# Kernel tuning notes

Measured on AMD Instinct MI355X. Metric: run time of the kernel, lower is better.

The kernel has to match this reference:

```python
import jax, jax.numpy as jnp
import numpy as np
from jax import lax

B, H7, W24 = 2048, 7, 24

def _conv(x, w):
    # x: [B,Cin,H,W], w: [Cout,Cin,3,3], stride 1, SAME padding (= padding 1)
    return lax.conv_general_dilated(x, w, (1, 1), 'SAME',
                                    dimension_numbers=('NCHW', 'OIHW', 'NCHW'))

def _cell(x, h, c, Wx, bx, Wh, Wc):
    # Wx: [4H,Cin,3,3] (gates i,f,c,o fused), Wh: [4H,H,3,3], Wc: [3,1,H,Hh,Ww] peepholes (i,f,o)
    H = h.shape[1]
    g = _conv(x, Wx) + bx[None, :, None, None] + _conv(h, Wh)  # [B,4H,Hh,Ww]
    gi, gf, gc, go = jnp.split(g, 4, axis=1)
    ci = jax.nn.sigmoid(gi + c * Wc[0])
    cf = jax.nn.sigmoid(gf + c * Wc[1])
    cc = cf * c + ci * jnp.tanh(gc)
    co = jax.nn.sigmoid(go + cc * Wc[2])
    ch = co * jnp.tanh(cc)
    return ch, cc

def setup_inputs() -> dict:
    key = jax.random.key(0)
    ks = jax.random.split(key, 12)
    s = 0.05
    return {
        'input': jax.random.normal(ks[0], (B, 2, H7, W24), jnp.float32),
        'x_ex': jax.random.normal(ks[1], (B, W24), jnp.float32),
        'Wx0': jax.random.normal(ks[2], (128, 2, 3, 3), jnp.float32) * s,
        'bx0': jax.random.normal(ks[3], (128,), jnp.float32) * s,
        'Wh0': jax.random.normal(ks[4], (128, 32, 3, 3), jnp.float32) * s,
        'Wc0': jnp.zeros((3, 1, 32, H7, W24), jnp.float32),
        'Wx1': jax.random.normal(ks[5], (256, 32, 3, 3), jnp.float32) * s,
        'bx1': jax.random.normal(ks[6], (256,), jnp.float32) * s,
        'Wh1': jax.random.normal(ks[7], (256, 64, 3, 3), jnp.float32) * s,
        'Wc1': jnp.zeros((3, 1, 64, H7, W24), jnp.float32),
        'fc1_w': jax.random.normal(ks[8], (64, 64 * H7 * W24), jnp.float32) * s,
        'fc1_b': jax.random.normal(ks[9], (64,), jnp.float32) * s,
        'exfc_w': jax.random.normal(ks[10], (64, W24), jnp.float32) * s,
        'exfc_b': jax.random.normal(ks[11], (64,), jnp.float32) * s,
    }

def reference(input, x_ex, Wx0, bx0, Wh0, Wc0, Wx1, bx1, Wh1, Wc1,
              fc1_w, fc1_b, exfc_w, exfc_b):
    b = input.shape[0]
    z0 = jnp.zeros((b, 32, H7, W24), input.dtype)
    z1 = jnp.zeros((b, 64, H7, W24), input.dtype)

    def step_fn(carry, _):
        h0, c0, h1, c1 = carry
        h0, c0 = _cell(input, h0, c0, Wx0, bx0, Wh0, Wc0)
        h1, c1 = _cell(h0, h1, c1, Wx1, bx1, Wh1, Wc1)
        return (h0, c0, h1, c1), None

    (h0, c0, h1, c1), _ = lax.scan(step_fn, (z0, z0, z1, z1), None, length=7)
    # last effective-step output is the top-layer hidden state after step 7
    h1f = jax.nn.relu(h1.reshape(b, -1) @ fc1_w.T + fc1_b)
    hex_ = jax.nn.relu(x_ex @ exfc_w.T + exfc_b)
    return jnp.concatenate((h1f, hex_), axis=1)  # [B,128]
```

## Files before the change

kernel.cpp:

```cpp
#include <hip/hip_runtime.h>
#include <math.h>


typedef __bf16 bf16x8 __attribute__((ext_vector_type(8)));
typedef float  f32x4  __attribute__((ext_vector_type(4)));

__device__ __forceinline__ float sigm(float x)  { return 1.f / (1.f + __expf(-x)); }
__device__ __forceinline__ float ftanh(float x) { float e = __expf(2.f * x); return 1.f - 2.f / (e + 1.f); }
__device__ __forceinline__ unsigned short bf16b(float x) {
  __bf16 h = (__bf16)x; unsigned short u; __builtin_memcpy(&u, &h, 2); return u;
}
__device__ __forceinline__ __bf16 ub2bf(unsigned short u) {
  __bf16 h; __builtin_memcpy(&h, &u, 2); return h;
}

#define OFF_WP0  ((size_t)0)
#define OFF_WP1  ((size_t)81920)
#define OFF_WFC  ((size_t)524288)
#define WS_NEED  ((size_t)1900544)

#define SH0N 9360
#define SH1N 16848
#define SX2N 5376

__global__ void pack_w0(const float* __restrict__ wx0, const float* __restrict__ wh0,
                        const float* __restrict__ bx0, __bf16* __restrict__ dst) {
  int o = blockIdx.x * 256 + threadIdx.x;
  if (o >= 40960) return;
  int e = o & 7, L = (o >> 3) & 63;
  int idx = o >> 9;
  int g = idx & 3, sidx = idx >> 2;
  int s = sidx % 10, chh = sidx / 10;
  int n = g * 32 + chh * 16 + (L & 15);
  int k = s * 32 + (L >> 4) * 8 + e;
  float v = 0.f;
  if (k < 32) {
    if (k < 18) {
      int ky = k / 6, rem = k - ky * 6, kx = rem >> 1, ci = rem & 1;
      v = wx0[(n * 2 + ci) * 9 + ky * 3 + kx];
    } else if (k == 18) {
      v = bx0[n];
    }
  } else {
    int tk = k - 32, tap = tk >> 5, c = tk & 31;
    v = wh0[(n * 32 + c) * 9 + tap];
  }
  dst[o] = (__bf16)v;
}

__global__ void pack_w1(const float* __restrict__ wx1, const float* __restrict__ wh1,
                        __bf16* __restrict__ dst) {
  int o = blockIdx.x * 256 + threadIdx.x;
  if (o >= 221184) return;
  int e = o & 7, L = (o >> 3) & 63;
  int idx = o >> 9;
  int g = idx & 3, sidx = idx >> 2;
  int s = sidx % 27, chq = sidx / 27;
  int n = g * 64 + chq * 16 + (L & 15);
  int k = s * 32 + (L >> 4) * 8 + e;
  float v;
  if (k < 288) {
    int tap = k >> 5, c = k & 31;
    v = wx1[(n * 32 + c) * 9 + tap];
  } else {
    int tk = k - 288, s2 = tk >> 5, c = tk & 31, tap = s2 >> 1, hf = s2 & 1;
    v = wh1[(n * 64 + hf * 32 + c) * 9 + tap];
  }
  dst[o] = (__bf16)v;
}

__global__ void pack_wfc(const float* __restrict__ w, __bf16* __restrict__ dst) {
  int o = blockIdx.x * 256 + threadIdx.x;
  if (o >= 168 * 64 * 64) return;
  int pix = o >> 12, ch = (o >> 6) & 63, n = o & 63;
  dst[o] = (__bf16)w[n * 10752 + ch * 168 + pix];
}

__global__ __launch_bounds__(256, 2) void convlstm_persistent(
    const float* __restrict__ input, const float* __restrict__ x_ex,
    const __bf16* __restrict__ wp0, const __bf16* __restrict__ wp1,
    const __bf16* __restrict__ wfc2,
    const float* __restrict__ bx1,
    const float* __restrict__ wc0, const float* __restrict__ wc1,
    const float* __restrict__ fc1b,
    const float* __restrict__ exw, const float* __restrict__ exb,
    float* __restrict__ out)
{
  __shared__ __bf16 sh0[2 * SH0N];
  __shared__ __bf16 sh1[SH1N];
  __shared__ __bf16 sx2[SX2N];

  const int b = blockIdx.x;
  const int t = threadIdx.x;
  const int w = t >> 6, L = t & 63;
  const int lo16 = L & 15, hi4 = L >> 4;

  {
    int* p0 = (int*)sh0;
    for (int i = t; i < SH0N; i += 256) p0[i] = 0;
    int* p1 = (int*)sh1;
    for (int i = t; i < SH1N / 2; i += 256) p1[i] = 0;
    int* p2 = (int*)sx2;
    for (int i = t; i < SX2N / 2; i += 256) p2[i] = 0;
  }
  __syncthreads();

  if (t < 168) {
    int iy = t / 24, ix = t - iy * 24;
    __bf16* dst = sx2 + t * 32;
    for (int ky = 0; ky < 3; ++ky) {
      int y = iy + ky - 1;
      if (y < 0 || y >= 7) continue;
      for (int kx = 0; kx < 3; ++kx) {
        int x = ix + kx - 1;
        if (x < 0 || x >= 24) continue;
        int k0 = ky * 6 + kx * 2;
        dst[k0 + 0] = (__bf16)input[((b * 2 + 0) * 7 + y) * 24 + x];
        dst[k0 + 1] = (__bf16)input[((b * 2 + 1) * 7 + y) * 24 + x];
      }
    }
    dst[18] = (__bf16)1.0f;
  }

  const int mh = w >> 1, chh = w & 1;
  const int ch0 = chh * 16 + lo16;
  const int ch1 = w * 16 + lo16;

  const __bf16* w0f = wp0 + chh * 20480 + L * 8;
  const __bf16* w1f = wp1 + w * 55296 + L * 8;

  const float bi1 = bx1[ch1], bf1 = bx1[64 + ch1];
  const float bg1 = bx1[128 + ch1], bo1 = bx1[192 + ch1];

  float c0r[2][3][4];
#pragma unroll
  for (int q = 0; q < 2; ++q)
#pragma unroll
    for (int j = 0; j < 3; ++j)
#pragma unroll
      for (int r = 0; r < 4; ++r) c0r[q][j][r] = 0.f;

  float c1r[3][4][4];
#pragma unroll
  for (int p = 0; p < 3; ++p)
#pragma unroll
    for (int j = 0; j < 4; ++j)
#pragma unroll
      for (int r = 0; r < 4; ++r) c1r[p][j][r] = 0.f;

  __syncthreads();

#pragma unroll 1
  for (int st = 0; st < 7; ++st) {
    const __bf16* h0r = sh0 + (st & 1) * SH0N;
    __bf16*       h0w = sh0 + ((st + 1) & 1) * SH0N;

    unsigned h1d[3][4][2];

#pragma unroll
    for (int q = 0; q < 2; ++q) {
      const int tb = mh * 6 + q * 3;
      const int ntq = (mh == 1 && q == 1) ? 2 : 3;
      int b0h[3], b0x[3];
#pragma unroll
      for (int j = 0; j < 3; ++j) {
        int pr = (tb + j) * 16 + lo16;
        if (pr > 167) pr = 167;
        int iy = pr / 24, ix = pr - iy * 24;
        b0h[j] = (iy * 26 + ix) * 40;
        b0x[j] = pr * 32 + hi4 * 8;
      }
      f32x4 a0[4][3];
#pragma unroll
      for (int g = 0; g < 4; ++g)
#pragma unroll
        for (int j = 0; j < 3; ++j) a0[g][j] = (f32x4){0.f, 0.f, 0.f, 0.f};

      auto loadA0 = [&](int s, bf16x8* af) {
        if (s == 0) {
#pragma unroll
          for (int j = 0; j < 3; ++j) af[j] = *(const bf16x8*)(sx2 + b0x[j]);
        } else {
          int tap = s - 1, ky = tap / 3, kx = tap - ky * 3;
          int toff = (ky * 26 + kx) * 40 + hi4 * 8;
#pragma unroll
          for (int j = 0; j < 3; ++j) af[j] = *(const bf16x8*)(h0r + b0h[j] + toff);
        }
      };
      auto loadB0 = [&](int s, bf16x8* bc) {
#pragma unroll
        for (int g = 0; g < 4; ++g)
          bc[g] = *(const bf16x8*)(w0f + (s * 4 + g) * 512);
      };
      auto mfma0 = [&](bf16x8* af, bf16x8* bc) {
#pragma unroll
        for (int j = 0; j < 3; ++j)
#pragma unroll
          for (int g = 0; g < 4; ++g)
            a0[g][j] = __builtin_amdgcn_mfma_f32_16x16x32_bf16(af[j], bc[g], a0[g][j], 0, 0, 0);
      };

      bf16x8 afA[3], afB[3], bcA[4], bcB[4];
      loadA0(0, afA); loadB0(0, bcA);
      loadA0(1, afB); loadB0(1, bcB);
#pragma unroll 1
      for (int s = 0; s < 10; s += 2) {
        mfma0(afA, bcA);
        int s2 = (s + 2 < 10) ? s + 2 : 9;
        loadA0(s2, afA); loadB0(s2, bcA);
        mfma0(afB, bcB);
        int s3 = (s + 3 < 10) ? s + 3 : 9;
        loadA0(s3, afB); loadB0(s3, bcB);
      }

#pragma unroll
      for (int j = 0; j < 3; ++j) {
        int p0 = (tb + j) * 16 + hi4 * 4;
        if (j < ntq && p0 < 168) {
          const float* wpp = wc0 + ch0 * 168 + p0;
          f32x4 w_i = *(const f32x4*)(wpp);
          f32x4 w_f = *(const f32x4*)(wpp + 5376);
          f32x4 w_o = *(const f32x4*)(wpp + 10752);
#pragma unroll
          for (int r = 0; r < 4; ++r) {
            int p = p0 + r;
            float c = c0r[q][j][r];
            float gi = a0[0][j][r];
            float gf = a0[1][j][r];
            float gc = a0[2][j][r];
            float go = a0[3][j][r];
            float ig = sigm(gi + c * w_i[r]);
            float fg = sigm(gf + c * w_f[r]);
            float cn = fg * c + ig * ftanh(gc);
            float og = sigm(go + cn * w_o[r]);
            float hn = og * ftanh(cn);
            c0r[q][j][r] = cn;
            int iy = p / 24, ix = p - iy * 24;
            h0w[((iy + 1) * 26 + ix + 1) * 40 + ch0] = (__bf16)hn;
          }
        }
      }
    }
    __syncthreads();

#pragma unroll
    for (int p3 = 0; p3 < 3; ++p3) {
      const int ntp = (p3 == 2) ? 3 : 4;
      int b1h0[4], b1h1[4];
#pragma unroll
      for (int j = 0; j < 4; ++j) {
        int pr = (p3 * 4 + j) * 16 + lo16;
        if (pr > 167) pr = 167;
        int iy = pr / 24, ix = pr - iy * 24;
        b1h0[j] = (iy * 26 + ix) * 40;
        b1h1[j] = (iy * 26 + ix) * 72;
      }
      f32x4 a1[4][4];
#pragma unroll
      for (int g = 0; g < 4; ++g)
#pragma unroll
        for (int j = 0; j < 4; ++j) a1[g][j] = (f32x4){0.f, 0.f, 0.f, 0.f};

      auto loadA1 = [&](int s, bf16x8* af) {
        if (s < 9) {
          int ky = s / 3, kx = s - ky * 3;
          int toff = (ky * 26 + kx) * 40 + hi4 * 8;
#pragma unroll
          for (int j = 0; j < 4; ++j) af[j] = *(const bf16x8*)(h0w + b1h0[j] + toff);
        } else {
          int t2 = s - 9, tap = t2 >> 1, hf = t2 & 1;
          int ky = tap / 3, kx = tap - ky * 3;
          int toff = (ky * 26 + kx) * 72 + hf * 32 + hi4 * 8;
#pragma unroll
          for (int j = 0; j < 4; ++j) af[j] = *(const bf16x8*)(sh1 + b1h1[j] + toff);
        }
      };
      auto loadB1 = [&](int s, bf16x8* bc) {
#pragma unroll
        for (int g = 0; g < 4; ++g)
          bc[g] = *(const bf16x8*)(w1f + (s * 4 + g) * 512);
      };
      auto mfma1 = [&](bf16x8* af, bf16x8* bc) {
#pragma unroll
        for (int j = 0; j < 4; ++j) {
          if (j < ntp) {
#pragma unroll
            for (int g = 0; g < 4; ++g)
              a1[g][j] = __builtin_amdgcn_mfma_f32_16x16x32_bf16(af[j], bc[g], a1[g][j], 0, 0, 0);
          }
        }
      };

      bf16x8 af[4], bcA[4], bcB[4];
      loadB1(0, bcA); loadB1(1, bcB);
#pragma unroll 1
      for (int s = 0; s < 27; s += 2) {
        loadA1(s, af);
        mfma1(af, bcA);
        loadB1((s + 2 < 27) ? s + 2 : 26, bcA);
        if (s + 1 < 27) {
          loadA1(s + 1, af);
          mfma1(af, bcB);
          loadB1((s + 3 < 27) ? s + 3 : 26, bcB);
        }
      }

#pragma unroll
      for (int j = 0; j < 4; ++j) {
        int p0 = (p3 * 4 + j) * 16 + hi4 * 4;
        if (j < ntp && p0 < 168) {
          const float* wpp = wc1 + ch1 * 168 + p0;
          f32x4 w_i = *(const f32x4*)(wpp);
          f32x4 w_f = *(const f32x4*)(wpp + 10752);
          f32x4 w_o = *(const f32x4*)(wpp + 21504);
#pragma unroll
          for (int rp = 0; rp < 2; ++rp) {
            unsigned pk = 0;
#pragma unroll
            for (int h = 0; h < 2; ++h) {
              int r = rp * 2 + h;
              float c = c1r[p3][j][r];
              float gi = a1[0][j][r] + bi1;
              float gf = a1[1][j][r] + bf1;
              float gc = a1[2][j][r] + bg1;
              float go = a1[3][j][r] + bo1;
              float ig = sigm(gi + c * w_i[r]);
              float fg = sigm(gf + c * w_f[r]);
              float cn = fg * c + ig * ftanh(gc);
              float og = sigm(go + cn * w_o[r]);
              float hn = og * ftanh(cn);
              c1r[p3][j][r] = cn;
              pk |= (unsigned)bf16b(hn) << (h * 16);
            }
            h1d[p3][j][rp] = pk;
          }
        }
      }
    }
    __syncthreads();

#pragma unroll
    for (int p3 = 0; p3 < 3; ++p3) {
      const int ntp = (p3 == 2) ? 3 : 4;
#pragma unroll
      for (int j = 0; j < 4; ++j) {
        int p0 = (p3 * 4 + j) * 16 + hi4 * 4;
        if (j < ntp && p0 < 168) {
#pragma unroll
          for (int rp = 0; rp < 2; ++rp) {
            unsigned v = h1d[p3][j][rp];
#pragma unroll
            for (int h = 0; h < 2; ++h) {
              int p = p0 + rp * 2 + h;
              int iy = p / 24, ix = p - iy * 24;
              sh1[((iy + 1) * 26 + ix + 1) * 72 + ch1] =
                  ub2bf((unsigned short)(v >> (h * 16)));
            }
          }
        }
      }
    }
  }
  __syncthreads();

  {
    const __bf16* h1f = sh1;
    const int o = t & 3, pg = t >> 2;
    float part[16];
#pragma unroll
    for (int q = 0; q < 16; ++q) part[q] = 0.f;
#pragma unroll 1
    for (int jj = 0; jj < 3; ++jj) {
      int p = pg + 64 * jj;
      if (p < 168) {
        int iy = p / 24, ix = p - iy * 24;
        const __bf16* hrow = h1f + ((iy + 1) * 26 + ix + 1) * 72;
        const __bf16* wrow = wfc2 + (size_t)p * 4096 + o * 16;
        for (int ch = 0; ch < 64; ++ch) {
          float hv = (float)hrow[ch];
          bf16x8 wv0 = *(const bf16x8*)(wrow + ch * 64);
          bf16x8 wv1 = *(const bf16x8*)(wrow + ch * 64 + 8);
#pragma unroll
          for (int q = 0; q < 8; ++q) {
            part[q] += hv * (float)wv0[q];
            part[8 + q] += hv * (float)wv1[q];
          }
        }
      }
    }
    float* sacc = (float*)sh0;
    __syncthreads();
#pragma unroll
    for (int q = 0; q < 16; ++q) sacc[pg * 64 + o * 16 + q] = part[q];
    __syncthreads();
    if (t < 64) {
      float s = fc1b[t];
      for (int pg2 = 0; pg2 < 64; ++pg2) s += sacc[pg2 * 64 + t];
      out[(size_t)b * 128 + t] = fmaxf(s, 0.f);
    } else if (t < 128) {
      int j = t - 64;
      float s = exb[j];
      for (int k = 0; k < 24; ++k) s += x_ex[b * 24 + k] * exw[j * 24 + k];
      out[(size_t)b * 128 + 64 + j] = fmaxf(s, 0.f);
    }
  }
}

extern "C" void kernel_launch(void* const* d_in, const int* in_sizes, int n_in,
                              void* d_out, int out_size, void* d_ws, size_t ws_size,
                              hipStream_t stream) {
  const float* input = (const float*)d_in[0];
  const float* x_ex  = (const float*)d_in[1];
  const float* Wx0   = (const float*)d_in[2];
  const float* bx0   = (const float*)d_in[3];
  const float* Wh0   = (const float*)d_in[4];
  const float* Wc0   = (const float*)d_in[5];
  const float* Wx1   = (const float*)d_in[6];
  const float* bx1   = (const float*)d_in[7];
  const float* Wh1   = (const float*)d_in[8];
  const float* Wc1   = (const float*)d_in[9];
  const float* fc1w  = (const float*)d_in[10];
  const float* fc1b  = (const float*)d_in[11];
  const float* exw   = (const float*)d_in[12];
  const float* exb   = (const float*)d_in[13];
  (void)in_sizes; (void)n_in;

  if (ws_size < WS_NEED) {
    hipMemsetAsync(d_out, 0, (size_t)out_size * 4, stream);
    return;
  }

  char* ws = (char*)d_ws;
  __bf16* wp0  = (__bf16*)(ws + OFF_WP0);
  __bf16* wp1  = (__bf16*)(ws + OFF_WP1);
  __bf16* wfc2 = (__bf16*)(ws + OFF_WFC);

  pack_w0<<<160, 256, 0, stream>>>(Wx0, Wh0, bx0, wp0);
  pack_w1<<<864, 256, 0, stream>>>(Wx1, Wh1, wp1);
  pack_wfc<<<2688, 256, 0, stream>>>(fc1w, wfc2);

  convlstm_persistent<<<2048, 256, 0, stream>>>(
      input, x_ex, wp0, wp1, wfc2, bx1, Wc0, Wc1, fc1b, exw, exb,
      (float*)d_out);
}
```

Measured before the change: 2.169 ms.

## Shrink layer-1 pixel tiles, store peephole weights as bf16, fold bias into accumulators

Layer-1 gate computation now walks 4 groups of 3 pixel tiles instead of 3 groups of 4. This shrinks the live accumulator and A-fragment register sets so the kernel can fit the 2-blocks-per-CU launch bound with less spilling. Peephole weights are pre-packed to bf16 in a new small kernel, halving their global loads. The layer-1 bias is used as the initial accumulator value instead of being added afterwards. The trade-offs are more B-weight reloads per step, one extra pack launch, and peephole weights rounded to bf16.

```diff
diff --git a/kernel.cpp b/kernel.cpp
--- a/kernel.cpp
+++ b/kernel.cpp
@@ -3,6 +3,7 @@
 
 
 typedef __bf16 bf16x8 __attribute__((ext_vector_type(8)));
+typedef __bf16 bf16x4 __attribute__((ext_vector_type(4)));
 typedef float  f32x4  __attribute__((ext_vector_type(4)));
 
 __device__ __forceinline__ float sigm(float x)  { return 1.f / (1.f + __expf(-x)); }
@@ -17,7 +18,9 @@
 #define OFF_WP0  ((size_t)0)
 #define OFF_WP1  ((size_t)81920)
 #define OFF_WFC  ((size_t)524288)
-#define WS_NEED  ((size_t)1900544)
+#define OFF_WCP0 ((size_t)1900544)
+#define OFF_WCP1 ((size_t)1932800)
+#define WS_NEED  ((size_t)1997312)
 
 #define SH0N 9360
 #define SH1N 16848
@@ -76,12 +79,19 @@
   dst[o] = (__bf16)w[n * 10752 + ch * 168 + pix];
 }
 
+__global__ void pack_wc(const float* __restrict__ wc0, const float* __restrict__ wc1,
+                        __bf16* __restrict__ d0, __bf16* __restrict__ d1) {
+  int o = blockIdx.x * 256 + threadIdx.x;
+  if (o < 16128) d0[o] = (__bf16)wc0[o];
+  else if (o < 48384) d1[o - 16128] = (__bf16)wc1[o - 16128];
+}
+
 __global__ __launch_bounds__(256, 2) void convlstm_persistent(
     const float* __restrict__ input, const float* __restrict__ x_ex,
     const __bf16* __restrict__ wp0, const __bf16* __restrict__ wp1,
     const __bf16* __restrict__ wfc2,
     const float* __restrict__ bx1,
-    const float* __restrict__ wc0, const float* __restrict__ wc1,
+    const __bf16* __restrict__ wcp0, const __bf16* __restrict__ wcp1,
     const float* __restrict__ fc1b,
     const float* __restrict__ exw, const float* __restrict__ exb,
     float* __restrict__ out)
@@ -140,11 +150,11 @@
 #pragma unroll
       for (int r = 0; r < 4; ++r) c0r[q][j][r] = 0.f;
 
-  float c1r[3][4][4];
-#pragma unroll
-  for (int p = 0; p < 3; ++p)
-#pragma unroll
-    for (int j = 0; j < 4; ++j)
+  float c1r[4][3][4];
+#pragma unroll
+  for (int p = 0; p < 4; ++p)
+#pragma unroll
+    for (int j = 0; j < 3; ++j)
 #pragma unroll
       for (int r = 0; r < 4; ++r) c1r[p][j][r] = 0.f;
 
@@ -155,7 +165,7 @@
     const __bf16* h0r = sh0 + (st & 1) * SH0N;
     __bf16*       h0w = sh0 + ((st + 1) & 1) * SH0N;
 
-    unsigned h1d[3][4][2];
+    unsigned h1d[4][3][2];
 
 #pragma unroll
     for (int q = 0; q < 2; ++q) {
@@ -217,10 +227,10 @@
       for (int j = 0; j < 3; ++j) {
         int p0 = (tb + j) * 16 + hi4 * 4;
         if (j < ntq && p0 < 168) {
-          const float* wpp = wc0 + ch0 * 168 + p0;
-          f32x4 w_i = *(const f32x4*)(wpp);
-          f32x4 w_f = *(const f32x4*)(wpp + 5376);
-          f32x4 w_o = *(const f32x4*)(wpp + 10752);
+          const __bf16* wpp = wcp0 + ch0 * 168 + p0;
+          bf16x4 w_i = *(const bf16x4*)(wpp);
+          bf16x4 w_f = *(const bf16x4*)(wpp + 5376);
+          bf16x4 w_o = *(const bf16x4*)(wpp + 10752);
 #pragma unroll
           for (int r = 0; r < 4; ++r) {
             int p = p0 + r;
@@ -229,10 +239,10 @@
             float gf = a0[1][j][r];
             float gc = a0[2][j][r];
             float go = a0[3][j][r];
-            float ig = sigm(gi + c * w_i[r]);
-            float fg = sigm(gf + c * w_f[r]);
+            float ig = sigm(gi + c * (float)w_i[r]);
+            float fg = sigm(gf + c * (float)w_f[r]);
             float cn = fg * c + ig * ftanh(gc);
-            float og = sigm(go + cn * w_o[r]);
+            float og = sigm(go + cn * (float)w_o[r]);
             float hn = og * ftanh(cn);
             c0r[q][j][r] = cn;
             int iy = p / 24, ix = p - iy * 24;
@@ -244,35 +254,39 @@
     __syncthreads();
 
 #pragma unroll
-    for (int p3 = 0; p3 < 3; ++p3) {
-      const int ntp = (p3 == 2) ? 3 : 4;
-      int b1h0[4], b1h1[4];
-#pragma unroll
-      for (int j = 0; j < 4; ++j) {
-        int pr = (p3 * 4 + j) * 16 + lo16;
+    for (int p4 = 0; p4 < 4; ++p4) {
+      const int ntp = (p4 == 3) ? 2 : 3;
+      int b1h0[3], b1h1[3];
+#pragma unroll
+      for (int j = 0; j < 3; ++j) {
+        int pr = (p4 * 3 + j) * 16 + lo16;
         if (pr > 167) pr = 167;
         int iy = pr / 24, ix = pr - iy * 24;
         b1h0[j] = (iy * 26 + ix) * 40;
         b1h1[j] = (iy * 26 + ix) * 72;
       }
-      f32x4 a1[4][4];
-#pragma unroll
-      for (int g = 0; g < 4; ++g)
-#pragma unroll
-        for (int j = 0; j < 4; ++j) a1[g][j] = (f32x4){0.f, 0.f, 0.f, 0.f};
+      f32x4 a1[4][3];
+      {
+        const float binit[4] = {bi1, bf1, bg1, bo1};
+#pragma unroll
+        for (int g = 0; g < 4; ++g)
+#pragma unroll
+          for (int j = 0; j < 3; ++j)
+            a1[g][j] = (f32x4){binit[g], binit[g], binit[g], binit[g]};
+      }
 
       auto loadA1 = [&](int s, bf16x8* af) {
         if (s < 9) {
           int ky = s / 3, kx = s - ky * 3;
           int toff = (ky * 26 + kx) * 40 + hi4 * 8;
 #pragma unroll
-          for (int j = 0; j < 4; ++j) af[j] = *(const bf16x8*)(h0w + b1h0[j] + toff);
+          for (int j = 0; j < 3; ++j) af[j] = *(const bf16x8*)(h0w + b1h0[j] + toff);
         } else {
           int t2 = s - 9, tap = t2 >> 1, hf = t2 & 1;
           int ky = tap / 3, kx = tap - ky * 3;
           int toff = (ky * 26 + kx) * 72 + hf * 32 + hi4 * 8;
 #pragma unroll
-          for (int j = 0; j < 4; ++j) af[j] = *(const bf16x8*)(sh1 + b1h1[j] + toff);
+          for (int j = 0; j < 3; ++j) af[j] = *(const bf16x8*)(sh1 + b1h1[j] + toff);
         }
       };
       auto loadB1 = [&](int s, bf16x8* bc) {
@@ -282,7 +296,7 @@
       };
       auto mfma1 = [&](bf16x8* af, bf16x8* bc) {
 #pragma unroll
-        for (int j = 0; j < 4; ++j) {
+        for (int j = 0; j < 3; ++j) {
           if (j < ntp) {
 #pragma unroll
             for (int g = 0; g < 4; ++g)
@@ -291,7 +305,7 @@
         }
       };
 
-      bf16x8 af[4], bcA[4], bcB[4];
+      bf16x8 af[3], bcA[4], bcB[4];
       loadB1(0, bcA); loadB1(1, bcB);
 #pragma unroll 1
       for (int s = 0; s < 27; s += 2) {
@@ -306,33 +320,33 @@
       }
 
 #pragma unroll
-      for (int j = 0; j < 4; ++j) {
-        int p0 = (p3 * 4 + j) * 16 + hi4 * 4;
+      for (int j = 0; j < 3; ++j) {
+        int p0 = (p4 * 3 + j) * 16 + hi4 * 4;
         if (j < ntp && p0 < 168) {
-          const float* wpp = wc1 + ch1 * 168 + p0;
-          f32x4 w_i = *(const f32x4*)(wpp);
-          f32x4 w_f = *(const f32x4*)(wpp + 10752);
-          f32x4 w_o = *(const f32x4*)(wpp + 21504);
+          const __bf16* wpp = wcp1 + ch1 * 168 + p0;
+          bf16x4 w_i = *(const bf16x4*)(wpp);
+          bf16x4 w_f = *(const bf16x4*)(wpp + 10752);
+          bf16x4 w_o = *(const bf16x4*)(wpp + 21504);
 #pragma unroll
           for (int rp = 0; rp < 2; ++rp) {
             unsigned pk = 0;
 #pragma unroll
             for (int h = 0; h < 2; ++h) {
               int r = rp * 2 + h;
-              float c = c1r[p3][j][r];
-              float gi = a1[0][j][r] + bi1;
-              float gf = a1[1][j][r] + bf1;
-              float gc = a1[2][j][r] + bg1;
-              float go = a1[3][j][r] + bo1;
-              float ig = sigm(gi + c * w_i[r]);
-              float fg = sigm(gf + c * w_f[r]);
+              float c = c1r[p4][j][r];
+              float gi = a1[0][j][r];
+              float gf = a1[1][j][r];
+              float gc = a1[2][j][r];
+              float go = a1[3][j][r];
+              float ig = sigm(gi + c * (float)w_i[r]);
+              float fg = sigm(gf + c * (float)w_f[r]);
               float cn = fg * c + ig * ftanh(gc);
-              float og = sigm(go + cn * w_o[r]);
+              float og = sigm(go + cn * (float)w_o[r]);
               float hn = og * ftanh(cn);
-              c1r[p3][j][r] = cn;
+              c1r[p4][j][r] = cn;
               pk |= (unsigned)bf16b(hn) << (h * 16);
             }
-            h1d[p3][j][rp] = pk;
+            h1d[p4][j][rp] = pk;
           }
         }
       }
@@ -340,15 +354,15 @@
     __syncthreads();
 
 #pragma unroll
-    for (int p3 = 0; p3 < 3; ++p3) {
-      const int ntp = (p3 == 2) ? 3 : 4;
-#pragma unroll
-      for (int j = 0; j < 4; ++j) {
-        int p0 = (p3 * 4 + j) * 16 + hi4 * 4;
+    for (int p4 = 0; p4 < 4; ++p4) {
+      const int ntp = (p4 == 3) ? 2 : 3;
+#pragma unroll
+      for (int j = 0; j < 3; ++j) {
+        int p0 = (p4 * 3 + j) * 16 + hi4 * 4;
         if (j < ntp && p0 < 168) {
 #pragma unroll
           for (int rp = 0; rp < 2; ++rp) {
-            unsigned v = h1d[p3][j][rp];
+            unsigned v = h1d[p4][j][rp];
 #pragma unroll
             for (int h = 0; h < 2; ++h) {
               int p = p0 + rp * 2 + h;
@@ -434,12 +448,15 @@
   __bf16* wp0  = (__bf16*)(ws + OFF_WP0);
   __bf16* wp1  = (__bf16*)(ws + OFF_WP1);
   __bf16* wfc2 = (__bf16*)(ws + OFF_WFC);
+  __bf16* wcp0 = (__bf16*)(ws + OFF_WCP0);
+  __bf16* wcp1 = (__bf16*)(ws + OFF_WCP1);
 
   pack_w0<<<160, 256, 0, stream>>>(Wx0, Wh0, bx0, wp0);
   pack_w1<<<864, 256, 0, stream>>>(Wx1, Wh1, wp1);
   pack_wfc<<<2688, 256, 0, stream>>>(fc1w, wfc2);
+  pack_wc<<<189, 256, 0, stream>>>(Wc0, Wc1, wcp0, wcp1);
 
   convlstm_persistent<<<2048, 256, 0, stream>>>(
-      input, x_ex, wp0, wp1, wfc2, bx1, Wc0, Wc1, fc1b, exw, exb,
+      input, x_ex, wp0, wp1, wfc2, bx1, wcp0, wcp1, fc1b, exw, exb,
       (float*)d_out);
 }
```

Result: slower. 3.838 ms (+76.9%).
